# Kernel optimization log

Measured on AMD Instinct MI355X. Metric: run time of the kernel, lower is better.

Reference implementation:

```python
import jax, jax.numpy as jnp
import numpy as np

N = 50000      # number of graph nodes
D = 128        # in_dim == out_dim
R = 4          # num_ring
NNZ = 800000   # edges per ring (avg degree 16)


def setup_inputs() -> dict:
    key = jax.random.key(0)
    ks = jax.random.split(key, 12)
    s = 1.0 / np.sqrt(D)
    x = jax.random.normal(ks[0], (N, D), jnp.float32)
    W_self = jax.random.normal(ks[1], (D, D), jnp.float32) * s
    W_rings = jax.random.normal(ks[2], (R, D, D), jnp.float32) * s
    WC = jax.random.normal(ks[3], (D, D), jnp.float32) * s
    WD = jax.random.normal(ks[4], (D, D), jnp.float32) * s
    att_w = jax.random.normal(ks[5], (1, 2 * (R + 1) * D), jnp.float32) * s
    att_b = jnp.zeros((1,), jnp.float32)
    # degree^-0.5 style norms: positive, in (0, 1]
    out_deg_norm = jax.random.uniform(ks[6], (N, 1), jnp.float32, 0.05, 1.0)
    in_deg_norm = jax.random.uniform(ks[7], (N, 1), jnp.float32, 0.05, 1.0)
    rows = jax.random.randint(ks[8], (R, NNZ), 0, N, jnp.int32)
    cols = jax.random.randint(ks[9], (R, NNZ), 0, N, jnp.int32)
    return {"x": x, "W_self": W_self, "W_rings": W_rings, "WC": WC, "WD": WD,
            "att_w": att_w, "att_b": att_b, "out_deg_norm": out_deg_norm,
            "in_deg_norm": in_deg_norm, "rows": rows, "cols": cols}


def reference(x, W_self, W_rings, WC, WD, att_w, att_b, out_deg_norm, in_deg_norm, rows, cols):
    n, d = x.shape
    r = W_rings.shape[0]
    # ---- ring-wise sparse aggregation (dropout is identity at inference) ----
    z_self = x @ W_self.T                       # [N, D]
    z_list = [z_self]
    for i in range(r):
        h = (x @ W_rings[i].T) * out_deg_norm   # [N, D]
        # torch.sparse.mm(adj, h): out[row] += h[col] for each edge (row, col)
        z_i = jax.ops.segment_sum(h[cols[i]], rows[i], num_segments=n)
        z_list.append(z_i)
    z = jnp.concatenate(z_list, axis=1) * in_deg_norm   # [N, (R+1)*D]
    # ---- heterogeneous sensitivity interaction ----
    z3 = z.reshape(n, r + 1, d)                          # [N, R+1, D]
    z_hat_com = z3 @ WC                                  # [N, R+1, D]
    com_score = jnp.einsum('nrd,nsd->nrs', z_hat_com, z_hat_com)
    alpha_com = jax.nn.softmax(com_score, axis=-1)
    z_com = jnp.einsum('nrs,nsd->nrd', alpha_com, z_hat_com).reshape(n, -1)
    z_hat_dis = z3 @ WD                                  # [N, R+1, D]
    # pairwise differences: sub[n, r, s, :] = zd[n, r] - zd[n, s]
    sub = z_hat_dis[:, :, None, :] - z_hat_dis[:, None, :, :]   # [N, R+1, R+1, D]
    dis_score = jnp.einsum('nrd,nrsd->nrs', z_hat_dis, sub)
    alpha_dis = jax.nn.softmax(dis_score, axis=-1)
    z_dis = jnp.einsum('nrs,nrsd->nrd', alpha_dis, sub).reshape(n, -1)
    z_cat = jnp.concatenate([z_com, z_dis], axis=-1)     # [N, 2*(R+1)*D]
    beta = jax.nn.sigmoid(z_cat @ att_w.T + att_b)       # [N, 1]
    z_wave = beta * z_com + (1.0 - beta) * z_dis         # [N, (R+1)*D]
    return z_wave
```

## Files before the change

### kernel.cpp

```cpp
#include <hip/hip_runtime.h>
#include <hip/hip_bf16.h>

#define NN 50000
#define D 128
#define RR 4
#define NNZ 800000
#define NCHUNK 196

typedef float v2f    __attribute__((ext_vector_type(2)));
typedef float f32x4  __attribute__((ext_vector_type(4)));
typedef short bf16x8 __attribute__((ext_vector_type(8)));

static __device__ __forceinline__ unsigned short f2b(float f)
{
    __hip_bfloat16 h = __float2bfloat16(f);
    return *reinterpret_cast<unsigned short*>(&h);
}
static __device__ __forceinline__ float b2f(unsigned short u)
{
    union { unsigned u32; float f; } v; v.u32 = ((unsigned)u) << 16; return v.f;
}

__global__ __launch_bounds__(256) void hist_kernel(
    const int* __restrict__ rows, int* __restrict__ cnt)
{
    const int r = blockIdx.y;
    const int e = blockIdx.x * 256 + threadIdx.x;
    atomicAdd(&cnt[r * NN + rows[(size_t)r * NNZ + e]], 1);
}

__global__ __launch_bounds__(256) void scanA_kernel(
    const int* __restrict__ cnt, int* __restrict__ bsum)
{
    const int r = blockIdx.y, bx = blockIdx.x, t = threadIdx.x;
    const int idx = bx * 256 + t;
    int v = (idx < NN) ? cnt[r * NN + idx] : 0;
#pragma unroll
    for (int off = 32; off; off >>= 1) v += __shfl_xor(v, off);
    __shared__ int ws4[4];
    if ((t & 63) == 0) ws4[t >> 6] = v;
    __syncthreads();
    if (t == 0) bsum[r * NCHUNK + bx] = ws4[0] + ws4[1] + ws4[2] + ws4[3];
}

__global__ __launch_bounds__(256) void scanB_kernel(int* __restrict__ bsum)
{
    __shared__ int s[256];
    const int t = threadIdx.x;
    for (int r = 0; r < RR; ++r) {
        int v = (t < NCHUNK) ? bsum[r * NCHUNK + t] : 0;
        s[t] = v;
        __syncthreads();
        for (int off = 1; off < 256; off <<= 1) {
            int u = (t >= off) ? s[t - off] : 0;
            __syncthreads();
            s[t] += u;
            __syncthreads();
        }
        if (t < NCHUNK) bsum[r * NCHUNK + t] = s[t] - v;
        __syncthreads();
    }
}

__global__ __launch_bounds__(256) void scanC_kernel(
    const int* __restrict__ cnt, const int* __restrict__ bsum,
    int* __restrict__ rowptr, int* __restrict__ cursor)
{
    const int r = blockIdx.y, bx = blockIdx.x, t = threadIdx.x;
    const int idx = bx * 256 + t;
    int v = (idx < NN) ? cnt[r * NN + idx] : 0;
    __shared__ int s[256];
    s[t] = v;
    __syncthreads();
    for (int off = 1; off < 256; off <<= 1) {
        int u = (t >= off) ? s[t - off] : 0;
        __syncthreads();
        s[t] += u;
        __syncthreads();
    }
    const int excl = bsum[r * NCHUNK + bx] + s[t] - v;
    if (idx <= NN) rowptr[r * (NN + 1) + idx] = excl;
    if (idx < NN)  cursor[r * NN + idx] = excl;
}

__global__ __launch_bounds__(256) void fill_kernel(
    const int* __restrict__ rows, const int* __restrict__ cols,
    int* __restrict__ cursor, int* __restrict__ perm)
{
    const int r = blockIdx.y;
    const int e = blockIdx.x * 256 + threadIdx.x;
    const int row = rows[(size_t)r * NNZ + e];
    const int pos = atomicAdd(&cursor[r * NN + row], 1);
    perm[(size_t)r * NNZ + pos] = cols[(size_t)r * NNZ + e];
}

__global__ __launch_bounds__(256) void convw_kernel(
    const float* __restrict__ Wself, const float* __restrict__ Wrings,
    unsigned short* __restrict__ wh, unsigned short* __restrict__ wl)
{
    int idx = blockIdx.x * 256 + threadIdx.x;
    int jg = idx >> 7, k = idx & 127;
    float f = (jg < 128) ? Wself[(size_t)jg * 128 + k]
                         : Wrings[(size_t)(jg - 128) * 128 + k];
    unsigned short hi = f2b(f);
    wh[idx] = hi;
    wl[idx] = f2b(f - b2f(hi));
}

__global__ __launch_bounds__(256) void convt_kernel(
    const float* __restrict__ WC, const float* __restrict__ WD,
    unsigned short* __restrict__ wct_h, unsigned short* __restrict__ wct_l,
    unsigned short* __restrict__ wdt_h, unsigned short* __restrict__ wdt_l)
{
    int idx = blockIdx.x * 256 + threadIdx.x;
    int kk = idx >> 7, col = idx & 127;
    float c = WC[idx];
    float d = WD[idx];
    unsigned short ch = f2b(c), dh = f2b(d);
    wct_h[col * 128 + kk] = ch;
    wct_l[col * 128 + kk] = f2b(c - b2f(ch));
    wdt_h[col * 128 + kk] = dh;
    wdt_l[col * 128 + kk] = f2b(d - b2f(dh));
}

__global__ __launch_bounds__(256) void gemm_kernel(
    const float* __restrict__ x,
    const unsigned short* __restrict__ wh, const unsigned short* __restrict__ wl,
    const float* __restrict__ odn, float* __restrict__ out,
    float* __restrict__ h, int ct0, int nj, int ring0)
{
    const int t = threadIdx.x;
    const int w = t >> 6, l = t & 63;
    const int lr = l & 15, lk = l >> 4;
    const int n0 = blockIdx.x * 16;

    bf16x8 ah[4], al[4];
    const float* xr = x + (size_t)(n0 + lr) * D + lk * 8;
#pragma unroll
    for (int ks = 0; ks < 4; ++ks) {
        float4 v0 = *(const float4*)(xr + ks * 32);
        float4 v1 = *(const float4*)(xr + ks * 32 + 4);
        float f[8] = {v0.x, v0.y, v0.z, v0.w, v1.x, v1.y, v1.z, v1.w};
#pragma unroll
        for (int j = 0; j < 8; ++j) {
            unsigned short hi = f2b(f[j]);
            ah[ks][j] = (short)hi;
            al[ks][j] = (short)f2b(f[j] - b2f(hi));
        }
    }

    float od[4];
#pragma unroll
    for (int q = 0; q < 4; ++q) od[q] = odn[n0 + lk * 4 + q];

    for (int j = 0; j < nj; ++j) {
        const int ct = ct0 + w + 4 * j;
        const int colg = ct * 16 + lr;
        f32x4 acc = {0.f, 0.f, 0.f, 0.f};
#pragma unroll
        for (int ks = 0; ks < 4; ++ks) {
            bf16x8 bhv = *(const bf16x8*)&wh[(size_t)colg * D + ks * 32 + lk * 8];
            bf16x8 blv = *(const bf16x8*)&wl[(size_t)colg * D + ks * 32 + lk * 8];
            acc = __builtin_amdgcn_mfma_f32_16x16x32_bf16(ah[ks], bhv, acc, 0, 0, 0);
            acc = __builtin_amdgcn_mfma_f32_16x16x32_bf16(al[ks], bhv, acc, 0, 0, 0);
            acc = __builtin_amdgcn_mfma_f32_16x16x32_bf16(ah[ks], blv, acc, 0, 0, 0);
        }
        if (ct < 8) {
#pragma unroll
            for (int q = 0; q < 4; ++q) {
                int n = n0 + lk * 4 + q;
                out[(size_t)n * 640 + colg] = acc[q];
            }
        } else {
            const int r = (ct >> 3) - 1 - ring0;
            const int d = (ct & 7) * 16 + lr;
#pragma unroll
            for (int q = 0; q < 4; ++q) {
                int n = n0 + lk * 4 + q;
                h[((size_t)r * NN + n) * D + d] = acc[q] * od[q];
            }
        }
    }
}

__global__ __launch_bounds__(256) void gather_kernel(
    const float* __restrict__ h, const int* __restrict__ rp,
    const int* __restrict__ pm, float* __restrict__ z, int csr_base)
{
    const int hr = blockIdx.y;
    const int cr = hr + csr_base;
    const int ln = threadIdx.x & 63;
    const int row = blockIdx.x * 4 + (threadIdx.x >> 6);
    const int* rpr = rp + (size_t)cr * (NN + 1);
    const int s = rpr[row], e = rpr[row + 1];
    const float* hb = h + (size_t)hr * NN * D;
    const int* pmr = pm + (size_t)cr * NNZ;

    float2 acc = make_float2(0.f, 0.f);
    int i = s;
    for (; i + 4 <= e; i += 4) {
        int c0 = pmr[i], c1 = pmr[i + 1], c2 = pmr[i + 2], c3 = pmr[i + 3];
        float2 v0 = *(const float2*)&hb[(size_t)c0 * D + ln * 2];
        float2 v1 = *(const float2*)&hb[(size_t)c1 * D + ln * 2];
        float2 v2 = *(const float2*)&hb[(size_t)c2 * D + ln * 2];
        float2 v3 = *(const float2*)&hb[(size_t)c3 * D + ln * 2];
        acc.x += v0.x + v1.x + v2.x + v3.x;
        acc.y += v0.y + v1.y + v2.y + v3.y;
    }
    for (; i < e; ++i) {
        float2 v = *(const float2*)&hb[(size_t)pmr[i] * D + ln * 2];
        acc.x += v.x; acc.y += v.y;
    }
    *(float2*)&z[(size_t)row * 640 + (cr + 1) * 128 + ln * 2] = acc;
}

__device__ __forceinline__ int sidx(int r, int s)
{
    if (r > s) { int t = r; r = s; s = t; }
    return r * 5 + s - (r * (r + 1)) / 2;
}

__global__ __launch_bounds__(512, 4) void interact2_kernel(
    float* __restrict__ z,
    const unsigned short* __restrict__ wct_h, const unsigned short* __restrict__ wct_l,
    const unsigned short* __restrict__ wdt_h, const unsigned short* __restrict__ wdt_l,
    const float* __restrict__ att_w, const float* __restrict__ att_b,
    const float* __restrict__ idn)
{
    __shared__ float SB[2 * 5 * 16 * 128];

    const int t  = threadIdx.x;
    const int w  = t >> 6;
    const int l  = t & 63;
    const int lr = l & 15;
    const int lk = l >> 4;
    const int n0 = blockIdx.x * 16;

    const int mm = w >> 2;
    const int nq = w & 3;
    const unsigned short* bhp = mm ? wdt_h : wct_h;
    const unsigned short* blp = mm ? wdt_l : wct_l;

    f32x4 acc[5][2];
#pragma unroll
    for (int mt = 0; mt < 5; ++mt) {
        acc[mt][0] = (f32x4){0.f, 0.f, 0.f, 0.f};
        acc[mt][1] = (f32x4){0.f, 0.f, 0.f, 0.f};
    }

#pragma unroll
    for (int mt = 0; mt < 5; ++mt) {
        bf16x8 ah[4], al[4];
        const float* ap = z + (size_t)(n0 + lr) * 640 + mt * 128 + lk * 8;
#pragma unroll
        for (int ks = 0; ks < 4; ++ks) {
            float4 v0 = *(const float4*)(ap + ks * 32);
            float4 v1 = *(const float4*)(ap + ks * 32 + 4);
            float f[8] = {v0.x, v0.y, v0.z, v0.w, v1.x, v1.y, v1.z, v1.w};
#pragma unroll
            for (int j = 0; j < 8; ++j) {
                unsigned short hi = f2b(f[j]);
                ah[ks][j] = (short)hi;
                al[ks][j] = (short)f2b(f[j] - b2f(hi));
            }
        }
#pragma unroll
        for (int nt = 0; nt < 2; ++nt) {
            const int col = nq * 32 + nt * 16 + lr;
#pragma unroll
            for (int ks = 0; ks < 4; ++ks) {
                bf16x8 vh = *(const bf16x8*)&bhp[(size_t)col * 128 + ks * 32 + lk * 8];
                bf16x8 vl = *(const bf16x8*)&blp[(size_t)col * 128 + ks * 32 + lk * 8];
                acc[mt][nt] = __builtin_amdgcn_mfma_f32_16x16x32_bf16(ah[ks], vh, acc[mt][nt], 0, 0, 0);
                acc[mt][nt] = __builtin_amdgcn_mfma_f32_16x16x32_bf16(al[ks], vh, acc[mt][nt], 0, 0, 0);
                acc[mt][nt] = __builtin_amdgcn_mfma_f32_16x16x32_bf16(ah[ks], vl, acc[mt][nt], 0, 0, 0);
            }
        }
    }

#pragma unroll
    for (int mt = 0; mt < 5; ++mt)
#pragma unroll
        for (int nt = 0; nt < 2; ++nt) {
            const int col = nq * 32 + nt * 16 + lr;
#pragma unroll
            for (int q = 0; q < 4; ++q) {
                const int nd = lk * 4 + q;
                SB[(((mm * 5 + mt) * 16) + nd) * 128 + col] = acc[mt][nt][q];
            }
        }
    __syncthreads();

#pragma unroll
    for (int ii = 0; ii < 2; ++ii) {
        const int nd = w + ii * 8;
        const int n  = n0 + nd;
        const float nf = idn[n];

        v2f ar[5], dr[5];
#pragma unroll
        for (int r = 0; r < 5; ++r) {
            ar[r] = *(const v2f*)&SB[((r * 16) + nd) * 128 + 2 * l] * nf;
            dr[r] = *(const v2f*)&SB[(((5 + r) * 16) + nd) * 128 + 2 * l] * nf;
        }

        float pc[15], pd[15];
        {
            int k = 0;
#pragma unroll
            for (int r = 0; r < 5; ++r)
#pragma unroll
                for (int s = r; s < 5; ++s, ++k) {
                    v2f qc = ar[r] * ar[s];
                    v2f qd = dr[r] * dr[s];
                    float vc = qc.x + qc.y;
                    float vd = qd.x + qd.y;
#pragma unroll
                    for (int off = 32; off; off >>= 1) {
                        vc += __shfl_xor(vc, off);
                        vd += __shfl_xor(vd, off);
                    }
                    pc[k] = vc; pd[k] = vd;
                }
        }

        v2f zcom[5], zdis[5];
#pragma unroll
        for (int r = 0; r < 5; ++r) {
            float sc[5], m = -1e30f;
#pragma unroll
            for (int s = 0; s < 5; ++s) { sc[s] = pc[sidx(r, s)]; m = fmaxf(m, sc[s]); }
            float e[5], se = 0.f;
#pragma unroll
            for (int s = 0; s < 5; ++s) { e[s] = __expf(sc[s] - m); se += e[s]; }
            float inv = 1.f / se;
            v2f a2 = (v2f)0.f;
#pragma unroll
            for (int s = 0; s < 5; ++s) a2 += ar[s] * e[s];
            zcom[r] = a2 * inv;

            float qq = pd[sidx(r, r)];
            float sd[5], md = -1e30f;
#pragma unroll
            for (int s = 0; s < 5; ++s) { sd[s] = qq - pd[sidx(r, s)]; md = fmaxf(md, sd[s]); }
            float ed[5], sed = 0.f;
#pragma unroll
            for (int s = 0; s < 5; ++s) { ed[s] = __expf(sd[s] - md); sed += ed[s]; }
            float invd = 1.f / sed;
            v2f d2 = (v2f)0.f;
#pragma unroll
            for (int s = 0; s < 5; ++s) d2 += dr[s] * ed[s];
            zdis[r] = dr[r] - d2 * invd;
        }

        v2f p2 = (v2f)0.f;
#pragma unroll
        for (int r = 0; r < 5; ++r) {
            p2 += (*(const v2f*)&att_w[r * 128 + 2 * l]) * zcom[r];
            p2 += (*(const v2f*)&att_w[640 + r * 128 + 2 * l]) * zdis[r];
        }
        float part = p2.x + p2.y;
#pragma unroll
        for (int off = 32; off; off >>= 1) part += __shfl_xor(part, off);
        const float beta = 1.f / (1.f + __expf(-(part + att_b[0])));
        const float omb  = 1.f - beta;

#pragma unroll
        for (int r = 0; r < 5; ++r) {
            v2f o = zcom[r] * beta + zdis[r] * omb;
            *(v2f*)&z[(size_t)n * 640 + r * 128 + 2 * l] = o;
        }
    }
}

extern "C" void kernel_launch(void* const* d_in, const int* in_sizes, int n_in,
                              void* d_out, int out_size, void* d_ws, size_t ws_size,
                              hipStream_t stream)
{
    const float* x      = (const float*)d_in[0];
    const float* W_self = (const float*)d_in[1];
    const float* W_ring = (const float*)d_in[2];
    const float* WC     = (const float*)d_in[3];
    const float* WD     = (const float*)d_in[4];
    const float* att_w  = (const float*)d_in[5];
    const float* att_b  = (const float*)d_in[6];
    const float* odn    = (const float*)d_in[7];
    const float* idn    = (const float*)d_in[8];
    const int*   rows   = (const int*)d_in[9];
    const int*   cols   = (const int*)d_in[10];
    float* out = (float*)d_out;

    const size_t wb_sz  = (size_t)640 * 128 * 2;
    const size_t wt_sz  = (size_t)128 * 128 * 2;
    const size_t h1_sz  = (size_t)NN * D * 4;
    const size_t cnt_sz = (size_t)RR * NN * 4;
    const size_t rp_sz  = (size_t)RR * (NN + 1) * 4;
    const size_t cur_sz = (size_t)RR * NN * 4;
    const size_t bs_sz  = 4096;
    const size_t pm_sz  = (size_t)RR * NNZ * 4;
    const size_t fixed  = 2 * wb_sz + 4 * wt_sz + cnt_sz + rp_sz + cur_sz + bs_sz + pm_sz;
    const bool big = ws_size >= fixed + RR * h1_sz + 4096;

    char* p = (char*)d_ws;
    unsigned short* wh    = (unsigned short*)p; p += wb_sz;
    unsigned short* wl    = (unsigned short*)p; p += wb_sz;
    unsigned short* wct_h = (unsigned short*)p; p += wt_sz;
    unsigned short* wct_l = (unsigned short*)p; p += wt_sz;
    unsigned short* wdt_h = (unsigned short*)p; p += wt_sz;
    unsigned short* wdt_l = (unsigned short*)p; p += wt_sz;
    float* h    = (float*)p; p += (big ? RR : 1) * h1_sz;
    int* cnt    = (int*)p; p += cnt_sz;
    int* rowptr = (int*)p; p += rp_sz;
    int* cursor = (int*)p; p += cur_sz;
    int* bsum   = (int*)p; p += bs_sz;
    int* perm   = (int*)p;

    convw_kernel<<<320, 256, 0, stream>>>(W_self, W_ring, wh, wl);
    convt_kernel<<<64, 256, 0, stream>>>(WC, WD, wct_h, wct_l, wdt_h, wdt_l);

    hipMemsetAsync(cnt, 0, cnt_sz, stream);
    hist_kernel<<<dim3(NNZ / 256, RR), 256, 0, stream>>>(rows, cnt);
    scanA_kernel<<<dim3(NCHUNK, RR), 256, 0, stream>>>(cnt, bsum);
    scanB_kernel<<<1, 256, 0, stream>>>(bsum);
    scanC_kernel<<<dim3(NCHUNK, RR), 256, 0, stream>>>(cnt, bsum, rowptr, cursor);
    fill_kernel<<<dim3(NNZ / 256, RR), 256, 0, stream>>>(rows, cols, cursor, perm);

    if (big) {
        gemm_kernel<<<NN / 16, 256, 0, stream>>>(x, wh, wl, odn, out, h, 0, 10, 0);
        gather_kernel<<<dim3(NN / 4, RR), 256, 0, stream>>>(h, rowptr, perm, out, 0);
    } else {
        gemm_kernel<<<NN / 16, 256, 0, stream>>>(x, wh, wl, odn, out, h, 0, 2, 0);
        for (int r = 0; r < RR; ++r) {
            gemm_kernel<<<NN / 16, 256, 0, stream>>>(x, wh, wl, odn, out, h,
                                                     8 * (r + 1), 2, r);
            gather_kernel<<<dim3(NN / 4, 1), 256, 0, stream>>>(h, rowptr, perm, out, r);
        }
    }

    interact2_kernel<<<NN / 16, 512, 0, stream>>>(out, wct_h, wct_l, wdt_h, wdt_l,
                                                  att_w, att_b, idn);
}
```

Baseline: 1.158 ms.

## Aggregate raw features before ring projection instead of projecting then gathering

Uses linearity to reorder each ring's computation. Neighbour rows of x, scaled by out-degree norm, are gathered and summed first, and the ring weight matrix is applied afterwards. The projection result now goes straight into the output buffer, so the separate gemm pass that wrote h and the gather that read it back are removed. The gather now reads x and the norm instead of the precomputed h. Float summation order also changes, which can shift rounding slightly.

```diff
diff --git a/kernel.cpp b/kernel.cpp
--- a/kernel.cpp
+++ b/kernel.cpp
@@ -123,19 +123,57 @@
     wdt_l[col * 128 + kk] = f2b(d - b2f(dh));
 }
 
-__global__ __launch_bounds__(256) void gemm_kernel(
-    const float* __restrict__ x,
+__global__ __launch_bounds__(256) void gather2_kernel(
+    const float* __restrict__ x, const float* __restrict__ odn,
+    const int* __restrict__ rp, const int* __restrict__ pm,
+    float* __restrict__ y, int r0)
+{
+    const int cr = blockIdx.y + r0;
+    const int t = threadIdx.x;
+    const int row = blockIdx.x * 4 + (t >> 6);
+    const int l  = t & 63;
+    const int h  = l >> 5;
+    const int dq = l & 31;
+    const int* rpr = rp + (size_t)cr * (NN + 1);
+    const int s = rpr[row], e = rpr[row + 1];
+    const int* pmr = pm + (size_t)cr * NNZ;
+
+    f32x4 acc = {0.f, 0.f, 0.f, 0.f};
+    int i = s;
+    for (; i + 8 <= e; i += 8) {
+        int c0 = pmr[i + h],     c1 = pmr[i + 2 + h];
+        int c2 = pmr[i + 4 + h], c3 = pmr[i + 6 + h];
+        float o0 = odn[c0], o1 = odn[c1], o2 = odn[c2], o3 = odn[c3];
+        f32x4 v0 = *(const f32x4*)&x[(size_t)c0 * D + dq * 4];
+        f32x4 v1 = *(const f32x4*)&x[(size_t)c1 * D + dq * 4];
+        f32x4 v2 = *(const f32x4*)&x[(size_t)c2 * D + dq * 4];
+        f32x4 v3 = *(const f32x4*)&x[(size_t)c3 * D + dq * 4];
+        acc += v0 * o0 + v1 * o1 + v2 * o2 + v3 * o3;
+    }
+    for (; i + h < e; i += 2) {
+        int c = pmr[i + h];
+        acc += (*(const f32x4*)&x[(size_t)c * D + dq * 4]) * odn[c];
+    }
+#pragma unroll
+    for (int j = 0; j < 4; ++j) acc[j] += __shfl_xor(acc[j], 32);
+    if (h == 0)
+        *(f32x4*)&y[((size_t)blockIdx.y * NN + row) * D + dq * 4] = acc;
+}
+
+__global__ __launch_bounds__(256) void gemm5_kernel(
+    const float* __restrict__ x, const float* __restrict__ y,
     const unsigned short* __restrict__ wh, const unsigned short* __restrict__ wl,
-    const float* __restrict__ odn, float* __restrict__ out,
-    float* __restrict__ h, int ct0, int nj, int ring0)
-{
+    float* __restrict__ out, int s0, int r0)
+{
+    const int s = s0 + blockIdx.y;
+    const float* A = (s == 0) ? x : y + (size_t)(s - 1 - r0) * NN * D;
     const int t = threadIdx.x;
     const int w = t >> 6, l = t & 63;
     const int lr = l & 15, lk = l >> 4;
     const int n0 = blockIdx.x * 16;
 
     bf16x8 ah[4], al[4];
-    const float* xr = x + (size_t)(n0 + lr) * D + lk * 8;
+    const float* xr = A + (size_t)(n0 + lr) * D + lk * 8;
 #pragma unroll
     for (int ks = 0; ks < 4; ++ks) {
         float4 v0 = *(const float4*)(xr + ks * 32);
@@ -149,69 +187,25 @@
         }
     }
 
-    float od[4];
-#pragma unroll
-    for (int q = 0; q < 4; ++q) od[q] = odn[n0 + lk * 4 + q];
-
-    for (int j = 0; j < nj; ++j) {
-        const int ct = ct0 + w + 4 * j;
-        const int colg = ct * 16 + lr;
+#pragma unroll
+    for (int j = 0; j < 2; ++j) {
+        const int ctl = w + 4 * j;
+        const int jg  = s * 128 + ctl * 16 + lr;
         f32x4 acc = {0.f, 0.f, 0.f, 0.f};
 #pragma unroll
         for (int ks = 0; ks < 4; ++ks) {
-            bf16x8 bhv = *(const bf16x8*)&wh[(size_t)colg * D + ks * 32 + lk * 8];
-            bf16x8 blv = *(const bf16x8*)&wl[(size_t)colg * D + ks * 32 + lk * 8];
+            bf16x8 bhv = *(const bf16x8*)&wh[(size_t)jg * D + ks * 32 + lk * 8];
+            bf16x8 blv = *(const bf16x8*)&wl[(size_t)jg * D + ks * 32 + lk * 8];
             acc = __builtin_amdgcn_mfma_f32_16x16x32_bf16(ah[ks], bhv, acc, 0, 0, 0);
             acc = __builtin_amdgcn_mfma_f32_16x16x32_bf16(al[ks], bhv, acc, 0, 0, 0);
             acc = __builtin_amdgcn_mfma_f32_16x16x32_bf16(ah[ks], blv, acc, 0, 0, 0);
         }
-        if (ct < 8) {
-#pragma unroll
-            for (int q = 0; q < 4; ++q) {
-                int n = n0 + lk * 4 + q;
-                out[(size_t)n * 640 + colg] = acc[q];
-            }
-        } else {
-            const int r = (ct >> 3) - 1 - ring0;
-            const int d = (ct & 7) * 16 + lr;
-#pragma unroll
-            for (int q = 0; q < 4; ++q) {
-                int n = n0 + lk * 4 + q;
-                h[((size_t)r * NN + n) * D + d] = acc[q] * od[q];
-            }
-        }
-    }
-}
-
-__global__ __launch_bounds__(256) void gather_kernel(
-    const float* __restrict__ h, const int* __restrict__ rp,
-    const int* __restrict__ pm, float* __restrict__ z, int csr_base)
-{
-    const int hr = blockIdx.y;
-    const int cr = hr + csr_base;
-    const int ln = threadIdx.x & 63;
-    const int row = blockIdx.x * 4 + (threadIdx.x >> 6);
-    const int* rpr = rp + (size_t)cr * (NN + 1);
-    const int s = rpr[row], e = rpr[row + 1];
-    const float* hb = h + (size_t)hr * NN * D;
-    const int* pmr = pm + (size_t)cr * NNZ;
-
-    float2 acc = make_float2(0.f, 0.f);
-    int i = s;
-    for (; i + 4 <= e; i += 4) {
-        int c0 = pmr[i], c1 = pmr[i + 1], c2 = pmr[i + 2], c3 = pmr[i + 3];
-        float2 v0 = *(const float2*)&hb[(size_t)c0 * D + ln * 2];
-        float2 v1 = *(const float2*)&hb[(size_t)c1 * D + ln * 2];
-        float2 v2 = *(const float2*)&hb[(size_t)c2 * D + ln * 2];
-        float2 v3 = *(const float2*)&hb[(size_t)c3 * D + ln * 2];
-        acc.x += v0.x + v1.x + v2.x + v3.x;
-        acc.y += v0.y + v1.y + v2.y + v3.y;
-    }
-    for (; i < e; ++i) {
-        float2 v = *(const float2*)&hb[(size_t)pmr[i] * D + ln * 2];
-        acc.x += v.x; acc.y += v.y;
-    }
-    *(float2*)&z[(size_t)row * 640 + (cr + 1) * 128 + ln * 2] = acc;
+#pragma unroll
+        for (int q = 0; q < 4; ++q) {
+            int n = n0 + lk * 4 + q;
+            out[(size_t)n * 640 + jg] = acc[q];
+        }
+    }
 }
 
 __device__ __forceinline__ int sidx(int r, int s)
@@ -392,14 +386,14 @@
 
     const size_t wb_sz  = (size_t)640 * 128 * 2;
     const size_t wt_sz  = (size_t)128 * 128 * 2;
-    const size_t h1_sz  = (size_t)NN * D * 4;
+    const size_t y1_sz  = (size_t)NN * D * 4;
     const size_t cnt_sz = (size_t)RR * NN * 4;
     const size_t rp_sz  = (size_t)RR * (NN + 1) * 4;
     const size_t cur_sz = (size_t)RR * NN * 4;
     const size_t bs_sz  = 4096;
     const size_t pm_sz  = (size_t)RR * NNZ * 4;
     const size_t fixed  = 2 * wb_sz + 4 * wt_sz + cnt_sz + rp_sz + cur_sz + bs_sz + pm_sz;
-    const bool big = ws_size >= fixed + RR * h1_sz + 4096;
+    const bool big = ws_size >= fixed + RR * y1_sz + 4096;
 
     char* p = (char*)d_ws;
     unsigned short* wh    = (unsigned short*)p; p += wb_sz;
@@ -408,7 +402,7 @@
     unsigned short* wct_l = (unsigned short*)p; p += wt_sz;
     unsigned short* wdt_h = (unsigned short*)p; p += wt_sz;
     unsigned short* wdt_l = (unsigned short*)p; p += wt_sz;
-    float* h    = (float*)p; p += (big ? RR : 1) * h1_sz;
+    float* y    = (float*)p; p += (big ? RR : 1) * y1_sz;
     int* cnt    = (int*)p; p += cnt_sz;
     int* rowptr = (int*)p; p += rp_sz;
     int* cursor = (int*)p; p += cur_sz;
@@ -426,14 +420,13 @@
     fill_kernel<<<dim3(NNZ / 256, RR), 256, 0, stream>>>(rows, cols, cursor, perm);
 
     if (big) {
-        gemm_kernel<<<NN / 16, 256, 0, stream>>>(x, wh, wl, odn, out, h, 0, 10, 0);
-        gather_kernel<<<dim3(NN / 4, RR), 256, 0, stream>>>(h, rowptr, perm, out, 0);
+        gather2_kernel<<<dim3(NN / 4, RR), 256, 0, stream>>>(x, odn, rowptr, perm, y, 0);
+        gemm5_kernel<<<dim3(NN / 16, 5), 256, 0, stream>>>(x, y, wh, wl, out, 0, 0);
     } else {
-        gemm_kernel<<<NN / 16, 256, 0, stream>>>(x, wh, wl, odn, out, h, 0, 2, 0);
+        gemm5_kernel<<<dim3(NN / 16, 1), 256, 0, stream>>>(x, y, wh, wl, out, 0, 0);
         for (int r = 0; r < RR; ++r) {
-            gemm_kernel<<<NN / 16, 256, 0, stream>>>(x, wh, wl, odn, out, h,
-                                                     8 * (r + 1), 2, r);
-            gather_kernel<<<dim3(NN / 4, 1), 256, 0, stream>>>(h, rowptr, perm, out, r);
+            gather2_kernel<<<dim3(NN / 4, 1), 256, 0, stream>>>(x, odn, rowptr, perm, y, r);
+            gemm5_kernel<<<dim3(NN / 16, 1), 256, 0, stream>>>(x, y, wh, wl, out, r + 1, r);
         }
     }
 
```

Result: no change. 1.176 ms (+1.6%).
